# Kernel optimization log

Measured on AMD Instinct MI355X. Metric: run time of the kernel, lower is better.

The kernel has to match this reference:

```python
import jax, jax.numpy as jnp
import numpy as np

H = 16  # num_attention_heads


def setup_inputs() -> dict:
    key = jax.random.key(0)
    k1, k2, k3 = jax.random.split(key, 3)
    B, S, E = 2, 2048, 1024
    return {
        "hidden_states": jax.random.normal(k1, (B, S, E), dtype=jnp.float32),
        "W_attn": jax.random.normal(k2, (E, 3 * E), dtype=jnp.float32) * 0.02,
        "b_attn": jnp.zeros((3 * E,), dtype=jnp.float32),
        "W_proj": jax.random.normal(k3, (E, E), dtype=jnp.float32) * 0.02,
        "b_proj": jnp.zeros((E,), dtype=jnp.float32),
    }


def reference(hidden_states, W_attn, b_attn, W_proj, b_proj):
    B, S, E = hidden_states.shape
    hd = E // H
    # Conv1D: x @ W + b -> [B, S, 3E]
    qkv = hidden_states @ W_attn + b_attn
    # Faithful to module: _split_heads with 3*head_dim FIRST, then split q/k/v.
    # i.e. per-head slice of size 3*hd is [q_h | k_h | v_h] (interleaved layout).
    qkv = qkv.reshape(B, S, H, 3 * hd).transpose(0, 2, 1, 3)  # [B, H, S, 3*hd]
    q, k, v = jnp.split(qkv, 3, axis=-1)                      # each [B, H, S, hd]
    # scores, scaled by sqrt(head_dim) (value.size(-1) ** 0.5)
    scores = jnp.einsum("bhqd,bhkd->bhqk", q, k) / jnp.asarray(hd, q.dtype) ** 0.5
    # causal mask via where with masked_bias = -10000.0 (not -inf), as in module
    causal = jnp.tril(jnp.ones((S, S), dtype=bool))
    scores = jnp.where(causal, scores, jnp.asarray(-10000.0, scores.dtype))
    attn_weights = jax.nn.softmax(scores, axis=-1)  # dropout p=0 -> identity
    attn_out = jnp.einsum("bhqk,bhkd->bhqd", attn_weights, v)
    attn_out = attn_out.transpose(0, 2, 1, 3).reshape(B, S, E)  # merge heads
    return attn_out @ W_proj + b_proj
```

## Files before the change

### kernel.cpp

```cpp
#include <hip/hip_runtime.h>
#include <hip/hip_bf16.h>


typedef __attribute__((ext_vector_type(4))) float f32x4;
typedef __attribute__((ext_vector_type(8))) short short8;
typedef __attribute__((ext_vector_type(2))) unsigned int uint2v;

#define AS1 __attribute__((address_space(1)))
#define AS3 __attribute__((address_space(3)))

__device__ __forceinline__ void load_lds16(const void* g, void* l) {
    __builtin_amdgcn_global_load_lds((const AS1 void*)g, (AS3 void*)l, 16, 0, 0);
}

__device__ __forceinline__ unsigned short f2bf(float f) {
    union { float f; unsigned int u; } v; v.f = f;
    unsigned int r = v.u + 0x7FFFu + ((v.u >> 16) & 1u);
    return (unsigned short)(r >> 16);
}

__device__ __forceinline__ int cvt_pk_bf16(float lo, float hi) {
    int r;
    asm("v_cvt_pk_bf16_f32 %0, %1, %2" : "=v"(r) : "v"(lo), "v"(hi));
    return r;
}

__device__ __forceinline__ void transpose_tile(
    const float* __restrict__ W, unsigned short* __restrict__ Wt,
    int K, int N, int bx, int by, int t) {
    __shared__ float tile[32][33];
    int k0 = by * 32, n0 = bx * 32;
    int r = t >> 3, c = (t & 7) * 4;
    float4 v = *(const float4*)&W[(size_t)(k0 + r) * N + n0 + c];
    tile[r][c] = v.x; tile[r][c + 1] = v.y; tile[r][c + 2] = v.z; tile[r][c + 3] = v.w;
    __syncthreads();
    int n = t >> 3; int kk = (t & 7) * 4;
    ushort4 o;
    o.x = f2bf(tile[kk + 0][n]);
    o.y = f2bf(tile[kk + 1][n]);
    o.z = f2bf(tile[kk + 2][n]);
    o.w = f2bf(tile[kk + 3][n]);
    *(ushort4*)&Wt[(size_t)(n0 + n) * K + k0 + kk] = o;
}

__global__ __launch_bounds__(256) void prep(
    const float* __restrict__ hs, unsigned short* __restrict__ Xb,
    const float* __restrict__ W_attn, unsigned short* __restrict__ WaT,
    const float* __restrict__ W_proj, unsigned short* __restrict__ WpT) {
    int bid = blockIdx.x, t = threadIdx.x;
    if (bid < 4096) {
        int i = (bid * 256 + t) * 4;
        float4 v = *(const float4*)(hs + i);
        ushort4 o;
        o.x = f2bf(v.x); o.y = f2bf(v.y); o.z = f2bf(v.z); o.w = f2bf(v.w);
        *(ushort4*)(Xb + i) = o;
    } else if (bid < 7168) {
        int r = bid - 4096;
        transpose_tile(W_attn, WaT, 1024, 3072, r % 96, r / 96, t);
    } else {
        int r = bid - 7168;
        transpose_tile(W_proj, WpT, 1024, 1024, r % 32, r / 32, t);
    }
}

__global__ __launch_bounds__(256) void gemm_qkv(
    const unsigned short* __restrict__ A,
    const unsigned short* __restrict__ Bt,
    const float* __restrict__ bias,
    unsigned short* __restrict__ qk, unsigned short* __restrict__ Vt,
    int M, int N, int K) {
    __shared__ unsigned short Sh[8704];
    unsigned short* As = Sh;
    unsigned short* Bs = Sh + 4096;
    unsigned short* Tb = Sh;
    const int t = threadIdx.x, wave = t >> 6, lane = t & 63;
    const int l15 = lane & 15, quad = lane >> 4;
    const int m0 = blockIdx.y * 128, n0 = blockIdx.x * 128;
    const int srow = wave * 32 + (lane >> 2);
    const int sch = (lane & 3) * 8;
    const unsigned short* Ag = A + (size_t)(m0 + srow) * K + sch;
    const unsigned short* Bg = Bt + (size_t)(n0 + srow) * K + sch;
    unsigned short* AsW = &As[wave * 32 * 32];
    unsigned short* BsW = &Bs[wave * 32 * 32];
    const int wm = (wave >> 1) * 64, wn = (wave & 1) * 64;
    f32x4 acc[4][4] = {};
    for (int k0 = 0; k0 < K; k0 += 32) {
        load_lds16(Ag + k0, AsW);
        load_lds16(Ag + k0 + (size_t)16 * K, AsW + 16 * 32);
        load_lds16(Bg + k0, BsW);
        load_lds16(Bg + k0 + (size_t)16 * K, BsW + 16 * 32);
        __syncthreads();
        short8 af[4], bf[4];
#pragma unroll
        for (int i = 0; i < 4; ++i) {
            af[i] = *(const short8*)&As[(wm + i * 16 + l15) * 32 + quad * 8];
            bf[i] = *(const short8*)&Bs[(wn + i * 16 + l15) * 32 + quad * 8];
        }
#pragma unroll
        for (int mt = 0; mt < 4; ++mt)
#pragma unroll
            for (int nt = 0; nt < 4; ++nt)
                acc[mt][nt] = __builtin_amdgcn_mfma_f32_16x16x32_bf16(af[mt], bf[nt], acc[mt][nt], 0, 0, 0);
        __syncthreads();
    }
    const int rem = n0 % 192;
#pragma unroll
    for (int mt = 0; mt < 4; ++mt) {
        int mrow = m0 + wm + mt * 16 + quad * 4;
#pragma unroll
        for (int nt = 0; nt < 4; ++nt) {
            int col = n0 + wn + nt * 16 + l15;
            float bv = bias[col];
            int h = col / 192;
            int j = col - h * 192;
            if (j < 128) {
                float sc = (j < 64) ? 0.125f : 1.0f;
#pragma unroll
                for (int r = 0; r < 4; ++r)
                    qk[(size_t)(mrow + r) * 2048 + h * 128 + j] = f2bf((acc[mt][nt][r] + bv) * sc);
            } else {
                int d = j - 128;
                int s_local = wm + mt * 16 + quad * 4;
                ushort4 pk;
                pk.x = f2bf(acc[mt][nt][0] + bv);
                pk.y = f2bf(acc[mt][nt][1] + bv);
                pk.z = f2bf(acc[mt][nt][2] + bv);
                pk.w = f2bf(acc[mt][nt][3] + bv);
                *(ushort4*)&Tb[d * 136 + s_local] = pk;
            }
        }
    }
    if (rem != 0) {
        __syncthreads();
        int vhalf = (rem == 64) ? 1 : 0;
        int h = (n0 + vhalf * 64) / 192;
        int b = m0 >> 11;
        unsigned short* vbase = Vt + ((size_t)(b * 16 + h) * 64) * 2048 + (m0 & 2047);
        int drow = t >> 4, ch = (t & 15) * 8;
#pragma unroll
        for (int rr = 0; rr < 4; ++rr) {
            int d = rr * 16 + drow;
            *(uint4*)(vbase + (size_t)d * 2048 + ch) = *(const uint4*)&Tb[d * 136 + ch];
        }
    }
}

__global__ __launch_bounds__(256) void gemm_proj(
    const unsigned short* __restrict__ A,
    const unsigned short* __restrict__ Bt,
    const float* __restrict__ bias,
    float* __restrict__ C, int M, int N, int K) {
    __shared__ unsigned short As[128 * 32];
    __shared__ unsigned short Bs[64 * 32];
    const int t = threadIdx.x, wave = t >> 6, lane = t & 63;
    const int l15 = lane & 15, quad = lane >> 4;
    const int m0 = blockIdx.y * 128, n0 = blockIdx.x * 64;
    const int srowA = wave * 32 + (lane >> 2);
    const int sch = (lane & 3) * 8;
    const unsigned short* Ag = A + (size_t)(m0 + srowA) * K + sch;
    const unsigned short* Bg = Bt + (size_t)(n0 + wave * 16 + (lane >> 2)) * K + sch;
    unsigned short* AsW = &As[wave * 32 * 32];
    unsigned short* BsW = &Bs[wave * 16 * 32];
    const int wm = (wave >> 1) * 64, wn = (wave & 1) * 32;
    f32x4 acc[4][2] = {};
    for (int k0 = 0; k0 < K; k0 += 32) {
        load_lds16(Ag + k0, AsW);
        load_lds16(Ag + k0 + (size_t)16 * K, AsW + 16 * 32);
        load_lds16(Bg + k0, BsW);
        __syncthreads();
        short8 af[4], bf[2];
#pragma unroll
        for (int i = 0; i < 4; ++i)
            af[i] = *(const short8*)&As[(wm + i * 16 + l15) * 32 + quad * 8];
#pragma unroll
        for (int i = 0; i < 2; ++i)
            bf[i] = *(const short8*)&Bs[(wn + i * 16 + l15) * 32 + quad * 8];
#pragma unroll
        for (int mt = 0; mt < 4; ++mt)
#pragma unroll
            for (int nt = 0; nt < 2; ++nt)
                acc[mt][nt] = __builtin_amdgcn_mfma_f32_16x16x32_bf16(af[mt], bf[nt], acc[mt][nt], 0, 0, 0);
        __syncthreads();
    }
#pragma unroll
    for (int mt = 0; mt < 4; ++mt) {
        int mrow = m0 + wm + mt * 16 + quad * 4;
#pragma unroll
        for (int nt = 0; nt < 2; ++nt) {
            int col = n0 + wn + nt * 16 + l15;
            float bv = bias[col];
#pragma unroll
            for (int r = 0; r < 4; ++r)
                C[(size_t)(mrow + r) * N + col] = acc[mt][nt][r] + bv;
        }
    }
}

__device__ __forceinline__ void build_af(const int (&pk)[4][2], int qpar, short8 (&af)[2]) {
#pragma unroll
    for (int km = 0; km < 2; ++km) {
        uint2v r0 = __builtin_amdgcn_permlane32_swap(
            (unsigned)pk[2 * km][0], (unsigned)pk[2 * km + 1][0], false, false);
        uint2v r1 = __builtin_amdgcn_permlane32_swap(
            (unsigned)pk[2 * km][1], (unsigned)pk[2 * km + 1][1], false, false);
        int Ap0 = (int)r0[0], Bp0 = (int)r0[1];
        int Ap1 = (int)r1[0], Bp1 = (int)r1[1];
        int z0 = qpar ? Ap0 : Bp0;
        int z1 = qpar ? Ap1 : Bp1;
        int w0 = __builtin_amdgcn_ds_swizzle(z0, 0x401F);
        int w1 = __builtin_amdgcn_ds_swizzle(z1, 0x401F);
        int f0 = qpar ? w0 : Ap0, f1 = qpar ? w1 : Ap1;
        int g0 = qpar ? Bp0 : w0, g1 = qpar ? Bp1 : w1;
        int4 v = {f0, f1, g0, g1};
        af[km] = __builtin_bit_cast(short8, v);
    }
}

__global__ __launch_bounds__(256) void attn2(
    const unsigned short* __restrict__ qk,
    const unsigned short* __restrict__ Vt,
    unsigned short* __restrict__ out) {
    const int S = 2048;
    __shared__ unsigned short Ks[64][72];
    __shared__ unsigned short Vts[64][72];
    const int t = threadIdx.x, wave = t >> 6, lane = t & 63;
    const int l15 = lane & 15, quad = lane >> 4, qpar = quad & 1;
    const int bid = blockIdx.x;
    const int qt = (bid < 256) ? (15 - (bid >> 5)) : ((bid - 256) >> 5);
    const int bh = bid & 31;
    const int b = bh >> 4, h = bh & 15;
    const unsigned short* qkb = qk + (size_t)b * S * 2048 + h * 128;
    const unsigned short* vtb = Vt + (size_t)bh * 64 * 2048;

    const int q0 = qt * 128 + wave * 32;
    short8 qf[2][2];
#pragma unroll
    for (int sp = 0; sp < 2; ++sp) {
        int qr = q0 + sp * 16 + l15;
#pragma unroll
        for (int km = 0; km < 2; ++km)
            qf[sp][km] = *(const short8*)(qkb + (size_t)qr * 2048 + km * 32 + quad * 8);
    }
    f32x4 o0[4] = {}, o1[4] = {};
    float lr0 = 0.f, lr1 = 0.f;

    const int srow8 = t >> 3, chunk8 = (t & 7) * 8;
    const int vd = t >> 2, vch = (t & 3) * 8;
    const int KT = qt * 2 + 2;

    uint4 kreg0 = *(const uint4*)(qkb + (size_t)srow8 * 2048 + 64 + chunk8);
    uint4 kreg1 = *(const uint4*)(qkb + (size_t)(32 + srow8) * 2048 + 64 + chunk8);
    uint4 vreg0 = *(const uint4*)(vtb + (size_t)vd * 2048 + vch);
    uint4 vreg1 = *(const uint4*)(vtb + (size_t)vd * 2048 + vch + 32);

    const int qg0 = q0 + l15, qg1 = q0 + 16 + l15;
    const int q1max = q0 + 31;

    for (int kt = 0; kt < KT; ++kt) {
        __syncthreads();
        *(uint4*)&Ks[srow8][chunk8] = kreg0;
        *(uint4*)&Ks[32 + srow8][chunk8] = kreg1;
        *(uint4*)&Vts[vd][vch] = vreg0;
        *(uint4*)&Vts[vd][vch + 32] = vreg1;
        __syncthreads();
        if (kt + 1 < KT) {
            int kn = (kt + 1) * 64;
            kreg0 = *(const uint4*)(qkb + (size_t)(kn + srow8) * 2048 + 64 + chunk8);
            kreg1 = *(const uint4*)(qkb + (size_t)(kn + 32 + srow8) * 2048 + 64 + chunk8);
            vreg0 = *(const uint4*)(vtb + (size_t)vd * 2048 + kn + vch);
            vreg1 = *(const uint4*)(vtb + (size_t)vd * 2048 + kn + vch + 32);
        }
        const int kb = kt * 64;
        if (kb > q1max) continue;

        f32x4 s0[4] = {}, s1[4] = {};
        __builtin_amdgcn_s_setprio(1);
#pragma unroll
        for (int km = 0; km < 2; ++km)
#pragma unroll
            for (int nt = 0; nt < 4; ++nt) {
                short8 kf = *(const short8*)&Ks[nt * 16 + l15][km * 32 + quad * 8];
                s0[nt] = __builtin_amdgcn_mfma_f32_16x16x32_bf16(kf, qf[0][km], s0[nt], 0, 0, 0);
                s1[nt] = __builtin_amdgcn_mfma_f32_16x16x32_bf16(kf, qf[1][km], s1[nt], 0, 0, 0);
            }
        __builtin_amdgcn_s_setprio(0);

        const int ka = kb + quad * 4;
        if (kb + 63 > q0) {
#pragma unroll
            for (int nt = 0; nt < 4; ++nt)
#pragma unroll
                for (int r = 0; r < 4; ++r) {
                    if (ka + nt * 16 + r > qg0) s0[nt][r] = -1e30f;
                    if (ka + nt * 16 + r > qg1) s1[nt][r] = -1e30f;
                }
        }

        int pk0[4][2], pk1[4][2];
        float a0 = 0.f, a1 = 0.f;
#pragma unroll
        for (int nt = 0; nt < 4; ++nt) {
            float pa[4], pb[4];
#pragma unroll
            for (int r = 0; r < 4; ++r) {
                pa[r] = __expf(s0[nt][r]);
                pb[r] = __expf(s1[nt][r]);
                a0 += pa[r]; a1 += pb[r];
            }
            pk0[nt][0] = cvt_pk_bf16(pa[0], pa[1]);
            pk0[nt][1] = cvt_pk_bf16(pa[2], pa[3]);
            pk1[nt][0] = cvt_pk_bf16(pb[0], pb[1]);
            pk1[nt][1] = cvt_pk_bf16(pb[2], pb[3]);
        }
        lr0 += a0; lr1 += a1;

        short8 af0[2], af1[2];
        build_af(pk0, qpar, af0);
        build_af(pk1, qpar, af1);

        __builtin_amdgcn_s_setprio(1);
#pragma unroll
        for (int km = 0; km < 2; ++km)
#pragma unroll
            for (int nt = 0; nt < 4; ++nt) {
                short8 vf = *(const short8*)&Vts[nt * 16 + l15][km * 32 + quad * 8];
                o0[nt] = __builtin_amdgcn_mfma_f32_16x16x32_bf16(af0[km], vf, o0[nt], 0, 0, 0);
                o1[nt] = __builtin_amdgcn_mfma_f32_16x16x32_bf16(af1[km], vf, o1[nt], 0, 0, 0);
            }
        __builtin_amdgcn_s_setprio(0);
    }

    float t0 = lr0 + __shfl_xor(lr0, 16);
    t0 += __shfl_xor(t0, 32);
    float t1 = lr1 + __shfl_xor(lr1, 16);
    t1 += __shfl_xor(t1, 32);
    unsigned short* ob = out + (size_t)b * S * 1024 + h * 64;
#pragma unroll
    for (int r = 0; r < 4; ++r) {
        float i0 = 1.0f / __shfl(t0, quad * 4 + r);
        float i1 = 1.0f / __shfl(t1, quad * 4 + r);
        size_t r0 = (size_t)(q0 + quad * 4 + r) * 1024;
        size_t r1 = (size_t)(q0 + 16 + quad * 4 + r) * 1024;
#pragma unroll
        for (int nt = 0; nt < 4; ++nt) {
            ob[r0 + nt * 16 + l15] = f2bf(o0[nt][r] * i0);
            ob[r1 + nt * 16 + l15] = f2bf(o1[nt][r] * i1);
        }
    }
}

extern "C" void kernel_launch(void* const* d_in, const int* in_sizes, int n_in,
                              void* d_out, int out_size, void* d_ws, size_t ws_size,
                              hipStream_t stream) {
    const float* hs     = (const float*)d_in[0];
    const float* W_attn = (const float*)d_in[1];
    const float* b_attn = (const float*)d_in[2];
    const float* W_proj = (const float*)d_in[3];
    const float* b_proj = (const float*)d_in[4];
    float* out = (float*)d_out;

    const int B = 2, S = 2048, E = 1024;
    const int M = B * S;
    const int N3 = 3 * E;

    unsigned short* Xb  = (unsigned short*)d_ws;
    unsigned short* WaT = Xb + (size_t)M * E;
    unsigned short* WpT = WaT + (size_t)N3 * E;
    unsigned short* qkb = WpT + (size_t)E * E;
    unsigned short* Vt  = qkb + (size_t)M * 2048;
    unsigned short* ao  = Vt + (size_t)M * E;

    prep<<<dim3(8192), 256, 0, stream>>>(hs, Xb, W_attn, WaT, W_proj, WpT);

    gemm_qkv<<<dim3(N3 / 128, M / 128), 256, 0, stream>>>(Xb, WaT, b_attn, qkb, Vt, M, N3, E);

    attn2<<<dim3(512), 256, 0, stream>>>(qkb, Vt, ao);

    gemm_proj<<<dim3(E / 64, M / 128), 256, 0, stream>>>(ao, WpT, b_proj, out, M, E, E);
}
```

Before: 195.9 us.

## Split attention query tile across eight waves with double-buffered K/V LDS

The attention kernel now launches 512 threads per block, with each wave owning 16 query rows instead of 32, so each wave holds half as many accumulators and scores. K and V tiles are double-buffered in shared memory, which removes the leading barrier per iteration, and each thread loads one K and one V chunk per tile instead of two. This aims to raise occupancy and hide latency better, at the cost of K/V fragment reads from LDS being shared by fewer query rows per wave and a larger per-block shared-memory footprint.

```diff
diff --git a/kernel.cpp b/kernel.cpp
--- a/kernel.cpp
+++ b/kernel.cpp
@@ -216,13 +216,13 @@
     }
 }
 
-__global__ __launch_bounds__(256) void attn2(
+__global__ __launch_bounds__(512, 4) void attn3(
     const unsigned short* __restrict__ qk,
     const unsigned short* __restrict__ Vt,
     unsigned short* __restrict__ out) {
     const int S = 2048;
-    __shared__ unsigned short Ks[64][72];
-    __shared__ unsigned short Vts[64][72];
+    __shared__ unsigned short Ks[2][64][72];
+    __shared__ unsigned short Vts[2][64][72];
     const int t = threadIdx.x, wave = t >> 6, lane = t & 63;
     const int l15 = lane & 15, quad = lane >> 4, qpar = quad & 1;
     const int bid = blockIdx.x;
@@ -232,120 +232,95 @@
     const unsigned short* qkb = qk + (size_t)b * S * 2048 + h * 128;
     const unsigned short* vtb = Vt + (size_t)bh * 64 * 2048;
 
-    const int q0 = qt * 128 + wave * 32;
-    short8 qf[2][2];
-#pragma unroll
-    for (int sp = 0; sp < 2; ++sp) {
-        int qr = q0 + sp * 16 + l15;
-#pragma unroll
-        for (int km = 0; km < 2; ++km)
-            qf[sp][km] = *(const short8*)(qkb + (size_t)qr * 2048 + km * 32 + quad * 8);
-    }
-    f32x4 o0[4] = {}, o1[4] = {};
-    float lr0 = 0.f, lr1 = 0.f;
+    const int q0 = qt * 128 + wave * 16;
+    short8 qf[2];
+#pragma unroll
+    for (int km = 0; km < 2; ++km)
+        qf[km] = *(const short8*)(qkb + (size_t)(q0 + l15) * 2048 + km * 32 + quad * 8);
+    f32x4 o[4] = {};
+    float lrun = 0.f;
 
     const int srow8 = t >> 3, chunk8 = (t & 7) * 8;
-    const int vd = t >> 2, vch = (t & 3) * 8;
     const int KT = qt * 2 + 2;
 
-    uint4 kreg0 = *(const uint4*)(qkb + (size_t)srow8 * 2048 + 64 + chunk8);
-    uint4 kreg1 = *(const uint4*)(qkb + (size_t)(32 + srow8) * 2048 + 64 + chunk8);
-    uint4 vreg0 = *(const uint4*)(vtb + (size_t)vd * 2048 + vch);
-    uint4 vreg1 = *(const uint4*)(vtb + (size_t)vd * 2048 + vch + 32);
-
-    const int qg0 = q0 + l15, qg1 = q0 + 16 + l15;
-    const int q1max = q0 + 31;
+    uint4 kreg = *(const uint4*)(qkb + (size_t)srow8 * 2048 + 64 + chunk8);
+    uint4 vreg = *(const uint4*)(vtb + (size_t)srow8 * 2048 + chunk8);
+
+    const int qg = q0 + l15;
+    const int qmax = q0 + 15;
 
     for (int kt = 0; kt < KT; ++kt) {
-        __syncthreads();
-        *(uint4*)&Ks[srow8][chunk8] = kreg0;
-        *(uint4*)&Ks[32 + srow8][chunk8] = kreg1;
-        *(uint4*)&Vts[vd][vch] = vreg0;
-        *(uint4*)&Vts[vd][vch + 32] = vreg1;
+        const int cur = kt & 1;
+        *(uint4*)&Ks[cur][srow8][chunk8] = kreg;
+        *(uint4*)&Vts[cur][srow8][chunk8] = vreg;
         __syncthreads();
         if (kt + 1 < KT) {
             int kn = (kt + 1) * 64;
-            kreg0 = *(const uint4*)(qkb + (size_t)(kn + srow8) * 2048 + 64 + chunk8);
-            kreg1 = *(const uint4*)(qkb + (size_t)(kn + 32 + srow8) * 2048 + 64 + chunk8);
-            vreg0 = *(const uint4*)(vtb + (size_t)vd * 2048 + kn + vch);
-            vreg1 = *(const uint4*)(vtb + (size_t)vd * 2048 + kn + vch + 32);
+            kreg = *(const uint4*)(qkb + (size_t)(kn + srow8) * 2048 + 64 + chunk8);
+            vreg = *(const uint4*)(vtb + (size_t)srow8 * 2048 + kn + chunk8);
         }
         const int kb = kt * 64;
-        if (kb > q1max) continue;
-
-        f32x4 s0[4] = {}, s1[4] = {};
+        if (kb > qmax) continue;
+
+        f32x4 s[4] = {};
         __builtin_amdgcn_s_setprio(1);
 #pragma unroll
         for (int km = 0; km < 2; ++km)
 #pragma unroll
             for (int nt = 0; nt < 4; ++nt) {
-                short8 kf = *(const short8*)&Ks[nt * 16 + l15][km * 32 + quad * 8];
-                s0[nt] = __builtin_amdgcn_mfma_f32_16x16x32_bf16(kf, qf[0][km], s0[nt], 0, 0, 0);
-                s1[nt] = __builtin_amdgcn_mfma_f32_16x16x32_bf16(kf, qf[1][km], s1[nt], 0, 0, 0);
+                short8 kf = *(const short8*)&Ks[cur][nt * 16 + l15][km * 32 + quad * 8];
+                s[nt] = __builtin_amdgcn_mfma_f32_16x16x32_bf16(kf, qf[km], s[nt], 0, 0, 0);
             }
         __builtin_amdgcn_s_setprio(0);
 
-        const int ka = kb + quad * 4;
         if (kb + 63 > q0) {
+            const int ka = kb + quad * 4;
 #pragma unroll
             for (int nt = 0; nt < 4; ++nt)
 #pragma unroll
-                for (int r = 0; r < 4; ++r) {
-                    if (ka + nt * 16 + r > qg0) s0[nt][r] = -1e30f;
-                    if (ka + nt * 16 + r > qg1) s1[nt][r] = -1e30f;
-                }
-        }
-
-        int pk0[4][2], pk1[4][2];
-        float a0 = 0.f, a1 = 0.f;
+                for (int r = 0; r < 4; ++r)
+                    if (ka + nt * 16 + r > qg) s[nt][r] = -1e30f;
+        }
+
+        int pk[4][2];
+        float a0 = 0.f;
 #pragma unroll
         for (int nt = 0; nt < 4; ++nt) {
-            float pa[4], pb[4];
+            float pa[4];
 #pragma unroll
             for (int r = 0; r < 4; ++r) {
-                pa[r] = __expf(s0[nt][r]);
-                pb[r] = __expf(s1[nt][r]);
-                a0 += pa[r]; a1 += pb[r];
+                pa[r] = __expf(s[nt][r]);
+                a0 += pa[r];
             }
-            pk0[nt][0] = cvt_pk_bf16(pa[0], pa[1]);
-            pk0[nt][1] = cvt_pk_bf16(pa[2], pa[3]);
-            pk1[nt][0] = cvt_pk_bf16(pb[0], pb[1]);
-            pk1[nt][1] = cvt_pk_bf16(pb[2], pb[3]);
-        }
-        lr0 += a0; lr1 += a1;
-
-        short8 af0[2], af1[2];
-        build_af(pk0, qpar, af0);
-        build_af(pk1, qpar, af1);
+            pk[nt][0] = cvt_pk_bf16(pa[0], pa[1]);
+            pk[nt][1] = cvt_pk_bf16(pa[2], pa[3]);
+        }
+        lrun += a0;
+
+        short8 af[2];
+        build_af(pk, qpar, af);
 
         __builtin_amdgcn_s_setprio(1);
 #pragma unroll
         for (int km = 0; km < 2; ++km)
 #pragma unroll
             for (int nt = 0; nt < 4; ++nt) {
-                short8 vf = *(const short8*)&Vts[nt * 16 + l15][km * 32 + quad * 8];
-                o0[nt] = __builtin_amdgcn_mfma_f32_16x16x32_bf16(af0[km], vf, o0[nt], 0, 0, 0);
-                o1[nt] = __builtin_amdgcn_mfma_f32_16x16x32_bf16(af1[km], vf, o1[nt], 0, 0, 0);
+                short8 vf = *(const short8*)&Vts[cur][nt * 16 + l15][km * 32 + quad * 8];
+                o[nt] = __builtin_amdgcn_mfma_f32_16x16x32_bf16(af[km], vf, o[nt], 0, 0, 0);
             }
         __builtin_amdgcn_s_setprio(0);
     }
 
-    float t0 = lr0 + __shfl_xor(lr0, 16);
+    float t0 = lrun + __shfl_xor(lrun, 16);
     t0 += __shfl_xor(t0, 32);
-    float t1 = lr1 + __shfl_xor(lr1, 16);
-    t1 += __shfl_xor(t1, 32);
     unsigned short* ob = out + (size_t)b * S * 1024 + h * 64;
 #pragma unroll
     for (int r = 0; r < 4; ++r) {
         float i0 = 1.0f / __shfl(t0, quad * 4 + r);
-        float i1 = 1.0f / __shfl(t1, quad * 4 + r);
         size_t r0 = (size_t)(q0 + quad * 4 + r) * 1024;
-        size_t r1 = (size_t)(q0 + 16 + quad * 4 + r) * 1024;
-#pragma unroll
-        for (int nt = 0; nt < 4; ++nt) {
-            ob[r0 + nt * 16 + l15] = f2bf(o0[nt][r] * i0);
-            ob[r1 + nt * 16 + l15] = f2bf(o1[nt][r] * i1);
-        }
+#pragma unroll
+        for (int nt = 0; nt < 4; ++nt)
+            ob[r0 + nt * 16 + l15] = f2bf(o[nt][r] * i0);
     }
 }
 
@@ -374,7 +349,7 @@
 
     gemm_qkv<<<dim3(N3 / 128, M / 128), 256, 0, stream>>>(Xb, WaT, b_attn, qkb, Vt, M, N3, E);
 
-    attn2<<<dim3(512), 256, 0, stream>>>(qkb, Vt, ao);
+    attn3<<<dim3(512), 512, 0, stream>>>(qkb, Vt, ao);
 
     gemm_proj<<<dim3(E / 64, M / 128), 256, 0, stream>>>(ao, WpT, b_proj, out, M, E, E);
 }
```

Measured after the change: 184.0 us. 6.0% less time.
